# Performance work log

Hardware: AMD Instinct MI355X
Metric: run time of the kernel (lower is better)

Reference implementation:

```python
import jax, jax.numpy as jnp
import numpy as np

# Dims: batch B, channels C, spatial HxW; modes: weight spatial (32, 17) ('count' mode)
B, C, H, W = 8, 128, 128, 128
M_ROWS, M_COLS = 32, 17          # weight spatial size = [n_modes[0], n_modes[1]//2 + 1]
L_TOP = 17                       # n_modes[0]//2 + 1  -> rows [:17]
R_BOT = 15                       # n_modes[0] - L_TOP -> rows [-15:]


def setup_inputs() -> dict:
    key = jax.random.key(0)
    k1, k2, k3 = jax.random.split(key, 3)
    scale = C ** (-2)  # matches torch: scale * rand(..., cfloat) -> re/im ~ U[0, scale)
    X = jax.random.normal(k1, (B, C, H, W), dtype=jnp.float32)
    linear_re = scale * jax.random.uniform(k2, (C, C, M_ROWS, M_COLS), dtype=jnp.float32)
    linear_im = scale * jax.random.uniform(k3, (C, C, M_ROWS, M_COLS), dtype=jnp.float32)
    return {"X": X, "linear_re": linear_re, "linear_im": linear_im}


def _block(w_eff, xf):
    # w_eff: (C, C, m0, m1) complex, xf: (B, C, m0, m1) complex -> (B, C, m0, m1)
    return jnp.einsum('ctxy,btxy->bcxy', w_eff, xf)


def reference(X, linear_re, linear_im):
    Wc = linear_re + 1j * linear_im                       # (C, C, 32, 17) complex64
    # skew-Hermitian weight: linear - conj(linear).transpose(1, 0)
    W_eff = Wc - jnp.conj(jnp.swapaxes(Wc, 0, 1))
    Xf = jnp.fft.rfftn(X, axes=(-2, -1), norm='forward')  # (B, C, H, W//2+1) complex
    Y = jnp.zeros(Xf.shape, dtype=jnp.complex64)
    # corner block 1: low positive row frequencies
    Y = Y.at[:, :, :L_TOP, :M_COLS].set(
        _block(W_eff[:, :, :L_TOP, :], Xf[:, :, :L_TOP, :M_COLS]))
    # corner block 2: negative row frequencies
    Y = Y.at[:, :, -R_BOT:, :M_COLS].set(
        _block(W_eff[:, :, -R_BOT:, :], Xf[:, :, -R_BOT:, :M_COLS]))
    out = jnp.fft.irfftn(Y, s=(H, W), axes=(-2, -1), norm='forward')
    return out.astype(X.dtype)
```

## Files before the change

kernel.cpp:

```cpp
#include <hip/hip_runtime.h>
#include <math.h>

#define PI_F 3.14159265358979323846f

constexpr int NM = 544;

__global__ __launch_bounds__(128) void k_fwd(const float* __restrict__ X,
                                             float2* __restrict__ Xf) {
  __shared__ float2 tw[128];
  __shared__ float2 tmp[17][129];
  const int y = threadIdx.x;
  {
    float s, c;
    sincosf(-2.0f * PI_F * (float)y / 128.0f, &s, &c);
    tw[y] = make_float2(c, s);
  }
  float2 acc[17];
#pragma unroll
  for (int r = 0; r < 17; ++r) acc[r] = make_float2(0.f, 0.f);
  __syncthreads();

  const float* xp = X + (size_t)blockIdx.x * 16384 + y;
  for (int x = 0; x < 128; ++x) {
    float v = xp[(size_t)x * 128];
    int j = 0;
#pragma unroll
    for (int r = 0; r < 17; ++r) {
      float2 w = tw[j];
      acc[r].x = fmaf(v, w.x, acc[r].x);
      acc[r].y = fmaf(v, w.y, acc[r].y);
      j = (j + x) & 127;
    }
  }
#pragma unroll
  for (int r = 0; r < 17; ++r) tmp[r][y] = acc[r];
  __syncthreads();

  float2* outp = Xf + (size_t)blockIdx.x * NM;
  for (int o = y; o < NM; o += 128) {
    int r = o / 17;
    int ky = o - r * 17;
    int r2 = (r < 17) ? r : (32 - r);
    float sgn = (r < 17) ? 1.f : -1.f;
    float zx = 0.f, zy = 0.f;
    int j = 0;
    for (int yy = 0; yy < 128; ++yy) {
      float2 v = tmp[r2][yy];
      float vy = v.y * sgn;
      float2 w = tw[j];
      zx += v.x * w.x - vy * w.y;
      zy += v.x * w.y + vy * w.x;
      j = (j + ky) & 127;
    }
    const float inv = 1.0f / 16384.0f;
    outp[o] = make_float2(zx * inv, zy * inv);
  }
}

__global__ __launch_bounds__(576) void k_mix(const float* __restrict__ Wre,
                                             const float* __restrict__ Wim,
                                             const float2* __restrict__ Xf,
                                             float2* __restrict__ Yp) {
  const int m = threadIdx.x;
  if (m >= NM) return;
  const int ct = blockIdx.x & 63;
  const int chunk = blockIdx.x >> 6;
  const int c0 = ct * 2;
  float ax[2][8], ay[2][8];
#pragma unroll
  for (int cc = 0; cc < 2; ++cc)
#pragma unroll
    for (int b = 0; b < 8; ++b) { ax[cc][b] = 0.f; ay[cc][b] = 0.f; }

  const int t0 = chunk * 32;
  for (int tt = 0; tt < 32; ++tt) {
    const int t = t0 + tt;
    float wr[2], wi[2];
#pragma unroll
    for (int cc = 0; cc < 2; ++cc) {
      const int c = c0 + cc;
      size_t ia = (size_t)(c * 128 + t) * NM + m;
      size_t ib = (size_t)(t * 128 + c) * NM + m;
      wr[cc] = Wre[ia] - Wre[ib];
      wi[cc] = Wim[ia] + Wim[ib];
    }
#pragma unroll
    for (int b = 0; b < 8; ++b) {
      float2 xv = Xf[(size_t)(b * 128 + t) * NM + m];
#pragma unroll
      for (int cc = 0; cc < 2; ++cc) {
        ax[cc][b] = fmaf(wr[cc], xv.x, fmaf(-wi[cc], xv.y, ax[cc][b]));
        ay[cc][b] = fmaf(wr[cc], xv.y, fmaf(wi[cc], xv.x, ay[cc][b]));
      }
    }
  }
#pragma unroll
  for (int b = 0; b < 8; ++b)
#pragma unroll
    for (int cc = 0; cc < 2; ++cc)
      Yp[(size_t)((chunk * 8 + b) * 128 + (c0 + cc)) * NM + m] =
          make_float2(ax[cc][b], ay[cc][b]);
}

__global__ __launch_bounds__(256) void k_inv(const float2* __restrict__ Yp,
                                             float* __restrict__ out) {
  __shared__ float2 Ys[NM];
  __shared__ float2 Z[128 * 17];
  __shared__ float2 tw[128];
  __shared__ float2 ctab[17][128];
  const int tid = threadIdx.x;
  const int b = blockIdx.x >> 7;
  const int c = blockIdx.x & 127;

  if (tid < 128) {
    float s, cc;
    sincosf(2.0f * PI_F * (float)tid / 128.0f, &s, &cc);
    tw[tid] = make_float2(cc, s);
  }
  for (int o = tid; o < 17 * 128; o += 256) {
    int ky = o >> 7, yy = o & 127;
    float s, cc;
    sincosf(2.0f * PI_F * (float)((ky * yy) & 127) / 128.0f, &s, &cc);
    float w = (ky == 0) ? 1.f : 2.f;
    ctab[ky][yy] = make_float2(w * cc, w * s);
  }
  for (int o = tid; o < NM; o += 256) {
    float sx = 0.f, sy = 0.f;
#pragma unroll
    for (int ch = 0; ch < 4; ++ch) {
      float2 v = Yp[(size_t)((ch * 8 + b) * 128 + c) * NM + o];
      sx += v.x; sy += v.y;
    }
    Ys[o] = make_float2(sx, sy);
  }
  __syncthreads();

  for (int o = tid; o < 128 * 17; o += 256) {
    int x = o / 17;
    int ky = o - x * 17;
    float zx = 0.f, zy = 0.f;
#pragma unroll
    for (int r = 0; r < 32; ++r) {
      int f = (r < 17) ? r : (r + 96);
      int j = (f * x) & 127;
      float2 Yv = Ys[r * 17 + ky];
      float2 w = tw[j];
      zx += Yv.x * w.x - Yv.y * w.y;
      zy += Yv.x * w.y + Yv.y * w.x;
    }
    Z[o] = make_float2(zx, zy);
  }
  __syncthreads();

  float* op = out + (size_t)blockIdx.x * 16384;
  for (int o = tid; o < 16384; o += 256) {
    int x = o >> 7, yy = o & 127;
    const float2* zr = &Z[x * 17];
    float s = 0.f;
#pragma unroll
    for (int ky = 0; ky < 17; ++ky) {
      float2 zv = zr[ky];
      float2 cv = ctab[ky][yy];
      s += zv.x * cv.x - zv.y * cv.y;
    }
    op[o] = s;
  }
}

extern "C" void kernel_launch(void* const* d_in, const int* in_sizes, int n_in,
                              void* d_out, int out_size, void* d_ws, size_t ws_size,
                              hipStream_t stream) {
  const float* X   = (const float*)d_in[0];
  const float* Wre = (const float*)d_in[1];
  const float* Wim = (const float*)d_in[2];
  float* out = (float*)d_out;

  float2* Xf = (float2*)d_ws;
  float2* Yp = Xf + (size_t)1024 * NM;

  k_fwd<<<dim3(1024), dim3(128), 0, stream>>>(X, Xf);
  k_mix<<<dim3(256), dim3(576), 0, stream>>>(Wre, Wim, Xf, Yp);
  k_inv<<<dim3(1024), dim3(256), 0, stream>>>(Yp, out);
}
```

Measured before the change: 350.7 us.

## Restructure spectral conv into table-driven DFT stages with split inverse kernels

Precomputes DFT twiddle tables in a new kernel and reads them from global memory instead of computing twiddle indices in the forward pass. The forward column DFT is re-partitioned across lanes and finished with a cross-half shuffle reduction. The mix kernel now handles one output channel per block with twice as many blocks. The inverse path is split into a reduction kernel, a row-inverse kernel and a column-inverse kernel, each keeping its twiddles in registers. This adds more launches and intermediate global traffic in exchange for more parallelism and simpler inner loops.

```diff
diff --git a/kernel.cpp b/kernel.cpp
--- a/kernel.cpp
+++ b/kernel.cpp
@@ -5,55 +5,104 @@
 
 constexpr int NM = 544;
 
+constexpr size_t OFF_F1 = 0;
+constexpr size_t OFF_F2 = 17408;
+constexpr size_t OFF_G  = 35840;
+constexpr size_t OFF_CT = 68608;
+constexpr size_t OFF_XF = 86016;
+constexpr size_t OFF_YS = 4542464;
+constexpr size_t OFF_YP = 8998912;
+
+__global__ __launch_bounds__(256) void k_tab(float* __restrict__ F1, float* __restrict__ F2,
+                                             float2* __restrict__ G, float2* __restrict__ CT) {
+  const int t0 = blockIdx.x * 256 + threadIdx.x;
+  const int N = gridDim.x * 256;
+  const float inv = 1.0f / 16384.0f;
+  for (int i = t0; i < 128 * 17; i += N) {
+    int x = i / 17, r = i - 17 * x;
+    float s, c; sincosf(-2.f * PI_F * (float)((x * r) & 127) / 128.f, &s, &c);
+    F1[x * 34 + 2 * r] = c * inv; F1[x * 34 + 2 * r + 1] = s * inv;
+  }
+  for (int i = t0; i < 128 * 18; i += N) {
+    int y = i / 18, k = i - 18 * y;
+    if (k == 17) { F2[y * 36 + 34] = 0.f; F2[y * 36 + 35] = 0.f; }
+    else {
+      float s, c; sincosf(-2.f * PI_F * (float)((y * k) & 127) / 128.f, &s, &c);
+      F2[y * 36 + 2 * k] = c; F2[y * 36 + 2 * k + 1] = s;
+    }
+  }
+  for (int i = t0; i < 32 * 128; i += N) {
+    int r = i >> 7, x = i & 127;
+    int f = (r < 17) ? r : r + 96;
+    float s, c; sincosf(2.f * PI_F * (float)((f * x) & 127) / 128.f, &s, &c);
+    G[i] = make_float2(c, s);
+  }
+  for (int i = t0; i < 17 * 128; i += N) {
+    int k = i >> 7;
+    float w = k ? 2.f : 1.f;
+    float s, c; sincosf(2.f * PI_F * (float)((k * (i & 127)) & 127) / 128.f, &s, &c);
+    CT[i] = make_float2(w * c, w * s);
+  }
+}
+
 __global__ __launch_bounds__(128) void k_fwd(const float* __restrict__ X,
+                                             const float* __restrict__ F1,
+                                             const float* __restrict__ F2,
                                              float2* __restrict__ Xf) {
-  __shared__ float2 tw[128];
-  __shared__ float2 tmp[17][129];
-  const int y = threadIdx.x;
-  {
-    float s, c;
-    sincosf(-2.0f * PI_F * (float)y / 128.0f, &s, &c);
-    tw[y] = make_float2(c, s);
-  }
+  __shared__ float2 tmp[128][17];
+  const int tid = threadIdx.x;
+  const int bt = blockIdx.x;
+
   float2 acc[17];
 #pragma unroll
   for (int r = 0; r < 17; ++r) acc[r] = make_float2(0.f, 0.f);
-  __syncthreads();
-
-  const float* xp = X + (size_t)blockIdx.x * 16384 + y;
+  const float* xp = X + (size_t)bt * 16384 + tid;
+#pragma unroll 4
   for (int x = 0; x < 128; ++x) {
     float v = xp[(size_t)x * 128];
-    int j = 0;
+    const float* f = F1 + x * 34;
 #pragma unroll
     for (int r = 0; r < 17; ++r) {
-      float2 w = tw[j];
-      acc[r].x = fmaf(v, w.x, acc[r].x);
-      acc[r].y = fmaf(v, w.y, acc[r].y);
-      j = (j + x) & 127;
-    }
-  }
-#pragma unroll
-  for (int r = 0; r < 17; ++r) tmp[r][y] = acc[r];
+      acc[r].x = fmaf(v, f[2 * r], acc[r].x);
+      acc[r].y = fmaf(v, f[2 * r + 1], acc[r].y);
+    }
+  }
+#pragma unroll
+  for (int r = 0; r < 17; ++r) tmp[tid][r] = acc[r];
   __syncthreads();
 
-  float2* outp = Xf + (size_t)blockIdx.x * NM;
-  for (int o = y; o < NM; o += 128) {
-    int r = o / 17;
-    int ky = o - r * 17;
-    int r2 = (r < 17) ? r : (32 - r);
-    float sgn = (r < 17) ? 1.f : -1.f;
-    float zx = 0.f, zy = 0.f;
-    int j = 0;
-    for (int yy = 0; yy < 128; ++yy) {
-      float2 v = tmp[r2][yy];
-      float vy = v.y * sgn;
-      float2 w = tw[j];
-      zx += v.x * w.x - vy * w.y;
-      zy += v.x * w.y + vy * w.x;
-      j = (j + ky) & 127;
-    }
-    const float inv = 1.0f / 16384.0f;
-    outp[o] = make_float2(zx * inv, zy * inv);
+  const int lane = tid & 63;
+  const int w = tid >> 6;
+  const int r = lane & 31;
+  const int yh = lane >> 5;
+  const int r2 = (r < 17) ? r : 32 - r;
+  const float sgn = (r < 17) ? 1.f : -1.f;
+  float2 a2[9];
+#pragma unroll
+  for (int i = 0; i < 9; ++i) a2[i] = make_float2(0.f, 0.f);
+  const float* f2b = F2 + w * 18 + yh * 36;
+  for (int yl = 0; yl < 64; ++yl) {
+    float2 tv = tmp[2 * yl + yh][r2];
+    float tvy = tv.y * sgn;
+    const float* f = f2b + yl * 72;
+#pragma unroll
+    for (int i = 0; i < 9; ++i) {
+      float cr = f[2 * i], ci = f[2 * i + 1];
+      a2[i].x = fmaf(tv.x, cr, fmaf(-tvy, ci, a2[i].x));
+      a2[i].y = fmaf(tv.x, ci, fmaf(tvy, cr, a2[i].y));
+    }
+  }
+#pragma unroll
+  for (int i = 0; i < 9; ++i) {
+    a2[i].x += __shfl_xor(a2[i].x, 32);
+    a2[i].y += __shfl_xor(a2[i].y, 32);
+  }
+  const int nky = w ? 8 : 9;
+  if (lane < 32) {
+    for (int i = 0; i < nky; ++i) {
+      int ky = w * 9 + i;
+      Xf[(size_t)bt * NM + r * 17 + ky] = a2[i];
+    }
   }
 }
 
@@ -63,107 +112,93 @@
                                              float2* __restrict__ Yp) {
   const int m = threadIdx.x;
   if (m >= NM) return;
-  const int ct = blockIdx.x & 63;
-  const int chunk = blockIdx.x >> 6;
-  const int c0 = ct * 2;
-  float ax[2][8], ay[2][8];
-#pragma unroll
-  for (int cc = 0; cc < 2; ++cc)
-#pragma unroll
-    for (int b = 0; b < 8; ++b) { ax[cc][b] = 0.f; ay[cc][b] = 0.f; }
-
+  const int c = blockIdx.x & 127;
+  const int chunk = blockIdx.x >> 7;
+  float2 acc[8];
+#pragma unroll
+  for (int b = 0; b < 8; ++b) acc[b] = make_float2(0.f, 0.f);
   const int t0 = chunk * 32;
+#pragma unroll 2
   for (int tt = 0; tt < 32; ++tt) {
     const int t = t0 + tt;
-    float wr[2], wi[2];
-#pragma unroll
-    for (int cc = 0; cc < 2; ++cc) {
-      const int c = c0 + cc;
-      size_t ia = (size_t)(c * 128 + t) * NM + m;
-      size_t ib = (size_t)(t * 128 + c) * NM + m;
-      wr[cc] = Wre[ia] - Wre[ib];
-      wi[cc] = Wim[ia] + Wim[ib];
-    }
+    float wr = Wre[(size_t)(c * 128 + t) * NM + m] - Wre[(size_t)(t * 128 + c) * NM + m];
+    float wi = Wim[(size_t)(c * 128 + t) * NM + m] + Wim[(size_t)(t * 128 + c) * NM + m];
 #pragma unroll
     for (int b = 0; b < 8; ++b) {
       float2 xv = Xf[(size_t)(b * 128 + t) * NM + m];
-#pragma unroll
-      for (int cc = 0; cc < 2; ++cc) {
-        ax[cc][b] = fmaf(wr[cc], xv.x, fmaf(-wi[cc], xv.y, ax[cc][b]));
-        ay[cc][b] = fmaf(wr[cc], xv.y, fmaf(wi[cc], xv.x, ay[cc][b]));
-      }
+      acc[b].x = fmaf(wr, xv.x, fmaf(-wi, xv.y, acc[b].x));
+      acc[b].y = fmaf(wr, xv.y, fmaf(wi, xv.x, acc[b].y));
     }
   }
 #pragma unroll
   for (int b = 0; b < 8; ++b)
-#pragma unroll
-    for (int cc = 0; cc < 2; ++cc)
-      Yp[(size_t)((chunk * 8 + b) * 128 + (c0 + cc)) * NM + m] =
-          make_float2(ax[cc][b], ay[cc][b]);
-}
-
-__global__ __launch_bounds__(256) void k_inv(const float2* __restrict__ Yp,
-                                             float* __restrict__ out) {
-  __shared__ float2 Ys[NM];
-  __shared__ float2 Z[128 * 17];
-  __shared__ float2 tw[128];
-  __shared__ float2 ctab[17][128];
+    Yp[(size_t)chunk * 1024 * NM + (size_t)(b * 128 + c) * NM + m] = acc[b];
+}
+
+__global__ __launch_bounds__(256) void k_red(const float2* __restrict__ Yp,
+                                             float2* __restrict__ Ys) {
+  int i = blockIdx.x * 256 + threadIdx.x;
+  if (i >= 1024 * NM) return;
+  int bc = i / NM, m = i - bc * NM;
+  int r = m / 17, ky = m - r * 17;
+  float2 s = make_float2(0.f, 0.f);
+#pragma unroll
+  for (int ch = 0; ch < 4; ++ch) {
+    float2 v = Yp[(size_t)ch * 1024 * NM + i];
+    s.x += v.x; s.y += v.y;
+  }
+  Ys[(size_t)bc * NM + ky * 32 + r] = s;
+}
+
+__global__ __launch_bounds__(256) void k_invB(const float* __restrict__ Ys,
+                                              const float2* __restrict__ G,
+                                              float2* __restrict__ Z) {
   const int tid = threadIdx.x;
-  const int b = blockIdx.x >> 7;
-  const int c = blockIdx.x & 127;
-
-  if (tid < 128) {
-    float s, cc;
-    sincosf(2.0f * PI_F * (float)tid / 128.0f, &s, &cc);
-    tw[tid] = make_float2(cc, s);
-  }
-  for (int o = tid; o < 17 * 128; o += 256) {
-    int ky = o >> 7, yy = o & 127;
-    float s, cc;
-    sincosf(2.0f * PI_F * (float)((ky * yy) & 127) / 128.0f, &s, &cc);
-    float w = (ky == 0) ? 1.f : 2.f;
-    ctab[ky][yy] = make_float2(w * cc, w * s);
-  }
-  for (int o = tid; o < NM; o += 256) {
-    float sx = 0.f, sy = 0.f;
-#pragma unroll
-    for (int ch = 0; ch < 4; ++ch) {
-      float2 v = Yp[(size_t)((ch * 8 + b) * 128 + c) * NM + o];
-      sx += v.x; sy += v.y;
-    }
-    Ys[o] = make_float2(sx, sy);
-  }
-  __syncthreads();
-
-  for (int o = tid; o < 128 * 17; o += 256) {
-    int x = o / 17;
-    int ky = o - x * 17;
-    float zx = 0.f, zy = 0.f;
+  const int lane = tid & 63;
+  const int bc = __builtin_amdgcn_readfirstlane(blockIdx.x * 2 + (tid >> 7));
+  const int xh = __builtin_amdgcn_readfirstlane((tid >> 6) & 1);
+  const int x = xh * 64 + lane;
+  float2 g[32];
+#pragma unroll
+  for (int r = 0; r < 32; ++r) g[r] = G[r * 128 + x];
+  const float* yb = Ys + (size_t)bc * (NM * 2);
+  float2* zb = Z + (size_t)bc * (17 * 128) + x;
+  for (int ky = 0; ky < 17; ++ky) {
+    const float* yk = yb + ky * 64;
+    float zr = 0.f, zi = 0.f;
 #pragma unroll
     for (int r = 0; r < 32; ++r) {
-      int f = (r < 17) ? r : (r + 96);
-      int j = (f * x) & 127;
-      float2 Yv = Ys[r * 17 + ky];
-      float2 w = tw[j];
-      zx += Yv.x * w.x - Yv.y * w.y;
-      zy += Yv.x * w.y + Yv.y * w.x;
-    }
-    Z[o] = make_float2(zx, zy);
-  }
-  __syncthreads();
-
-  float* op = out + (size_t)blockIdx.x * 16384;
-  for (int o = tid; o < 16384; o += 256) {
-    int x = o >> 7, yy = o & 127;
-    const float2* zr = &Z[x * 17];
+      float ar = yk[2 * r], ai = yk[2 * r + 1];
+      zr = fmaf(ar, g[r].x, fmaf(-ai, g[r].y, zr));
+      zi = fmaf(ar, g[r].y, fmaf(ai, g[r].x, zi));
+    }
+    zb[ky * 128] = make_float2(zr, zi);
+  }
+}
+
+__global__ __launch_bounds__(256) void k_invC(const float* __restrict__ Z,
+                                              const float2* __restrict__ CT,
+                                              float* __restrict__ out) {
+  const int tid = threadIdx.x;
+  const int yy = tid & 127;
+  const int xh = __builtin_amdgcn_readfirstlane(tid >> 7);
+  const int bc = blockIdx.x;
+  float2 ct[17];
+#pragma unroll
+  for (int k = 0; k < 17; ++k) ct[k] = CT[k * 128 + yy];
+  const float* zb = Z + (size_t)bc * (17 * 128 * 2);
+  float* op = out + (size_t)bc * 16384;
+#pragma unroll 2
+  for (int xi = 0; xi < 64; ++xi) {
+    int x = xh * 64 + xi;
+    const float* zp = zb + 2 * x;
     float s = 0.f;
 #pragma unroll
-    for (int ky = 0; ky < 17; ++ky) {
-      float2 zv = zr[ky];
-      float2 cv = ctab[ky][yy];
-      s += zv.x * cv.x - zv.y * cv.y;
-    }
-    op[o] = s;
+    for (int k = 0; k < 17; ++k) {
+      float zr = zp[k * 256], zi = zp[k * 256 + 1];
+      s = fmaf(zr, ct[k].x, fmaf(-zi, ct[k].y, s));
+    }
+    op[x * 128 + yy] = s;
   }
 }
 
@@ -175,10 +210,20 @@
   const float* Wim = (const float*)d_in[2];
   float* out = (float*)d_out;
 
-  float2* Xf = (float2*)d_ws;
-  float2* Yp = Xf + (size_t)1024 * NM;
-
-  k_fwd<<<dim3(1024), dim3(128), 0, stream>>>(X, Xf);
-  k_mix<<<dim3(256), dim3(576), 0, stream>>>(Wre, Wim, Xf, Yp);
-  k_inv<<<dim3(1024), dim3(256), 0, stream>>>(Yp, out);
-}
+  char* ws = (char*)d_ws;
+  float*  F1 = (float*)(ws + OFF_F1);
+  float*  F2 = (float*)(ws + OFF_F2);
+  float2* G  = (float2*)(ws + OFF_G);
+  float2* CT = (float2*)(ws + OFF_CT);
+  float2* Xf = (float2*)(ws + OFF_XF);
+  float2* Ys = (float2*)(ws + OFF_YS);
+  float2* Yp = (float2*)(ws + OFF_YP);
+  float2* Z  = Yp;
+
+  k_tab <<<32, 256, 0, stream>>>(F1, F2, G, CT);
+  k_fwd <<<1024, 128, 0, stream>>>(X, F1, F2, Xf);
+  k_mix <<<512, 576, 0, stream>>>(Wre, Wim, Xf, Yp);
+  k_red <<<2176, 256, 0, stream>>>(Yp, Ys);
+  k_invB<<<512, 256, 0, stream>>>((const float*)Ys, G, Z);
+  k_invC<<<1024, 256, 0, stream>>>((const float*)Z, CT, out);
+}
```

After: 345.0 us. About the same (-1.6%).
